# Kernel tuning notes

Measured on AMD Instinct MI355X. Metric: run time of the kernel, lower is better.

The kernel has to match this reference:

```python
import jax, jax.numpy as jnp
import numpy as np

# All unordered pairs of 6 ligand sites (octahedral complex)
PAIRS = np.array([(i, j) for i in range(6) for j in range(i + 1, 6)], dtype=np.int32)  # [15, 2]

B, N_LIGS, D = 32768, 6, 64
IN_DIM = D + 2 * D  # core + lig_i + lig_j = 192
H1, H2 = 64, 32


def setup_inputs() -> dict:
    key = jax.random.key(0)
    ks = jax.random.split(key, 8)
    s = 0.05  # small init scale for numerical sanity
    return {
        "core": jax.random.normal(ks[0], (B, D), dtype=jnp.float32),
        "ligs": jax.random.normal(ks[1], (B, N_LIGS, D), dtype=jnp.float32),
        "W1": jax.random.normal(ks[2], (IN_DIM, H1), dtype=jnp.float32) * s,
        "b1": jnp.zeros((H1,), dtype=jnp.float32),
        "W2": jax.random.normal(ks[3], (H1, H2), dtype=jnp.float32) * s,
        "b2": jnp.zeros((H2,), dtype=jnp.float32),
        "W3": jax.random.normal(ks[4], (H2, 1), dtype=jnp.float32) * s,
        "b3": jnp.zeros((1,), dtype=jnp.float32),
    }


def _mlp(x, W1, b1, W2, b2, W3, b3):
    # Dense(softplus) -> Dense(softplus) -> Dense(1, linear); dropout is identity at inference
    h = jax.nn.softplus(x @ W1 + b1)
    h = jax.nn.softplus(h @ W2 + b2)
    return h @ W3 + b3  # [..., 1]


def reference(core, ligs, W1, b1, W2, b2, W3, b3):
    i_idx = jnp.asarray(PAIRS[:, 0])
    j_idx = jnp.asarray(PAIRS[:, 1])
    P = PAIRS.shape[0]
    li = ligs[:, i_idx, :]  # [B, P, D]
    lj = ligs[:, j_idx, :]  # [B, P, D]
    c = jnp.broadcast_to(core[:, None, :], (core.shape[0], P, core.shape[1]))
    x1 = jnp.concatenate([c, li, lj], axis=-1)  # [B, P, 3D]
    x2 = jnp.concatenate([c, lj, li], axis=-1)  # [B, P, 3D]
    res = 0.5 * (_mlp(x1, W1, b1, W2, b2, W3, b3) + _mlp(x2, W1, b1, W2, b2, W3, b3))  # [B, P, 1]
    return jnp.sum(res, axis=1)  # [B, 1]
```

## Files before the change

### kernel.cpp

```cpp
#include <hip/hip_runtime.h>
#include <hip/hip_fp16.h>
#include <stdint.h>


typedef __attribute__((ext_vector_type(8))) _Float16 f16x8;
typedef __attribute__((ext_vector_type(2))) __fp16   fp16v2;
typedef __attribute__((ext_vector_type(4))) float    f32x4;
typedef __attribute__((ext_vector_type(4))) unsigned int u32x4;

constexpr int   BPB      = 64;
constexpr int   NT       = 1024;
constexpr int   T_STRIDE = 1680;
constexpr int   WT_RS    = 72;
constexpr int   WT_OFF   = BPB * T_STRIDE;
constexpr int   W2T_OFF  = WT_OFF + 192 * WT_RS * 2;
constexpr int   Y_OFF    = W2T_OFF + 32 * WT_RS * 2;
constexpr int   LDS_BYTES = Y_OFF + 256;

constexpr float L2E = 1.4426950408889634f;
constexpr float LN2 = 0.6931471805599453f;

constexpr unsigned long long I_BITS =
  (0ull<<0)|(0ull<<3)|(0ull<<6)|(0ull<<9)|(0ull<<12)|
  (1ull<<15)|(1ull<<18)|(1ull<<21)|(1ull<<24)|
  (2ull<<27)|(2ull<<30)|(2ull<<33)|
  (3ull<<36)|(3ull<<39)|(4ull<<42);
constexpr unsigned long long J_BITS =
  (1ull<<0)|(2ull<<3)|(3ull<<6)|(4ull<<9)|(5ull<<12)|
  (2ull<<15)|(3ull<<18)|(4ull<<21)|(5ull<<24)|
  (3ull<<27)|(4ull<<30)|(5ull<<33)|
  (4ull<<36)|(5ull<<39)|(5ull<<42);

__device__ __forceinline__ float sp2(float s) {
  float t = __builtin_amdgcn_exp2f(s);
  return __builtin_amdgcn_logf(1.0f + t);
}

__device__ __forceinline__ __half2 h1pair(__half2 u, __half2 a, __half2 b,
                                          __half2 one2) {
  __half2 s = __hadd2(__hadd2(u, a), b);
  __half2 t = h2exp2(s);
  return h2log2(__hadd2(one2, t));
}

__global__ __launch_bounds__(NT, 4)
void tb_fused(const float* __restrict__ core, const float* __restrict__ ligs,
              const float* __restrict__ W1,   const float* __restrict__ b1,
              const float* __restrict__ W2,   const float* __restrict__ b2,
              const float* __restrict__ W3,   const float* __restrict__ b3,
              float* __restrict__ out)
{
  extern __shared__ char smem[];
  const int tid  = (int)threadIdx.x;
  const int lane = tid & 63;
  const int ln   = lane & 15;
  const int qd   = lane >> 4;
  const int wv   = __builtin_amdgcn_readfirstlane(tid >> 6);
  const int qr   = wv >> 2;
  const int mtw  = wv & 3;
  const int b0   = (int)blockIdx.x * BPB;

  float* yred = (float*)(smem + Y_OFF);

  #pragma unroll 4
  for (int idx = tid; idx < 12288; idx += NT) {
    const int d = idx >> 6, n = idx & 63;
    *(uint16_t*)(smem + WT_OFF + ((((d >> 6) * 64 + n) * WT_RS + (d & 63)) * 2)) =
        __half_as_ushort(__float2half(W1[idx] * L2E));
  }
  #pragma unroll
  for (int idx = tid; idx < 2048; idx += NT) {
    const int k = idx >> 5, m = idx & 31;
    *(uint16_t*)(smem + W2T_OFF + ((m * WT_RS + k) * 2)) =
        __half_as_ushort(__float2half(W2[idx]));
  }
  if (tid < 64) yred[tid] = 0.0f;
  __syncthreads();

  #pragma unroll 1
  for (int rep = 0; rep < 2; ++rep) {
    const int xr = qr + rep * 4;
    if (xr >= 7) break;
    const float* src = (xr == 0)
        ? (core + (size_t)(b0 + mtw * 16 + ln) * 64)
        : (ligs + ((size_t)(b0 + mtw * 16 + ln) * 6 + (size_t)(xr - 1)) * 64);

    union AF { f16x8 v; fp16v2 p[4]; } Afr[2];
    #pragma unroll
    for (int ks = 0; ks < 2; ++ks) {
      const float4 f0 = *(const float4*)(src + ks * 32 + qd * 8);
      const float4 f1 = *(const float4*)(src + ks * 32 + qd * 8 + 4);
      Afr[ks].p[0] = __builtin_amdgcn_cvt_pkrtz(f0.x, f0.y);
      Afr[ks].p[1] = __builtin_amdgcn_cvt_pkrtz(f0.z, f0.w);
      Afr[ks].p[2] = __builtin_amdgcn_cvt_pkrtz(f1.x, f1.y);
      Afr[ks].p[3] = __builtin_amdgcn_cvt_pkrtz(f1.z, f1.w);
    }

    const int sl_lo = (xr == 0) ? 0 : 1;
    const int sl_hi = (xr == 0) ? 0 : 2;
    #pragma unroll 1
    for (int sl = sl_lo; sl <= sl_hi; ++sl) {
      const int trow = (xr == 0) ? 0 : ((sl == 1) ? xr : 6 + xr);
      #pragma unroll
      for (int nt = 0; nt < 4; ++nt) {
        f32x4 c = {0.f, 0.f, 0.f, 0.f};
        #pragma unroll
        for (int ks = 0; ks < 2; ++ks) {
          f16x8 Bf = *(const f16x8*)(smem + WT_OFF +
              (((sl * 64 + nt * 16 + ln) * WT_RS + ks * 32 + qd * 8) * 2));
          c = __builtin_amdgcn_mfma_f32_16x16x32_f16(Afr[ks].v, Bf, c, 0, 0, 0);
        }
        const float bias = (xr == 0) ? b1[nt * 16 + ln] * L2E : 0.0f;
        #pragma unroll
        for (int reg = 0; reg < 4; ++reg) {
          const int b = mtw * 16 + qd * 4 + reg;
          *(uint16_t*)(smem + (size_t)b * T_STRIDE + trow * 128 + (nt * 16 + ln) * 2) =
              __half_as_ushort(__float2half(c[reg] + bias));
        }
      }
    }
  }
  __syncthreads();

  f16x8 W2f[2][2];
  #pragma unroll
  for (int nt = 0; nt < 2; ++nt)
    #pragma unroll
    for (int ks = 0; ks < 2; ++ks)
      W2f[nt][ks] = *(const f16x8*)(smem + W2T_OFF +
          (((nt * 16 + ln) * WT_RS + ks * 32 + qd * 8) * 2));

  float b2v[2], w3v[2];
  #pragma unroll
  for (int nt = 0; nt < 2; ++nt) {
    b2v[nt] = b2[nt * 16 + ln] * L2E;
    w3v[nt] = W3[nt * 16 + ln] * LN2;
  }

  const __half2 one2 = __float2half2_rn(1.0f);
  const char* Tb  = smem + (size_t)(mtw * 16 + ln) * T_STRIDE;
  const int koff  = qd * 16;

  float yacc[4] = {0.f, 0.f, 0.f, 0.f};

  #pragma unroll 2
  for (int t3 = 0; t3 < 8; ++t3) {
    const int q = qr + 4 * t3;
    if (q >= 30) break;
    const int p  = q >> 1;
    const int iv = (int)((I_BITS >> (3 * p)) & 7ull);
    const int jv = (int)((J_BITS >> (3 * p)) & 7ull);
    const int An = (q & 1) ? jv : iv;
    const int Bn = (q & 1) ? iv : jv;
    const char* TA = Tb + (1 + An) * 128;
    const char* TB = Tb + (7 + Bn) * 128;

    union U4 { u32x4 u; __half2 h[4]; };
    U4 du0, da0, db0, du1, da1, db1;
    du0.u = *(const u32x4*)(Tb + koff);
    da0.u = *(const u32x4*)(TA + koff);
    db0.u = *(const u32x4*)(TB + koff);
    du1.u = *(const u32x4*)(Tb + 64 + koff);
    da1.u = *(const u32x4*)(TA + 64 + koff);
    db1.u = *(const u32x4*)(TB + 64 + koff);

    union { f16x8 v; __half2 h[4]; } A0, A1;
    #pragma unroll
    for (int w = 0; w < 4; ++w) A0.h[w] = h1pair(du0.h[w], da0.h[w], db0.h[w], one2);
    #pragma unroll
    for (int w = 0; w < 4; ++w) A1.h[w] = h1pair(du1.h[w], da1.h[w], db1.h[w], one2);

    f32x4 c0 = {0.f, 0.f, 0.f, 0.f};
    f32x4 c1 = {0.f, 0.f, 0.f, 0.f};
    c0 = __builtin_amdgcn_mfma_f32_16x16x32_f16(A0.v, W2f[0][0], c0, 0, 0, 0);
    c0 = __builtin_amdgcn_mfma_f32_16x16x32_f16(A1.v, W2f[0][1], c0, 0, 0, 0);
    c1 = __builtin_amdgcn_mfma_f32_16x16x32_f16(A0.v, W2f[1][0], c1, 0, 0, 0);
    c1 = __builtin_amdgcn_mfma_f32_16x16x32_f16(A1.v, W2f[1][1], c1, 0, 0, 0);

    #pragma unroll
    for (int reg = 0; reg < 4; ++reg) {
      yacc[reg] += sp2(c0[reg] + b2v[0]) * w3v[0]
                 + sp2(c1[reg] + b2v[1]) * w3v[1];
    }
  }

  #pragma unroll
  for (int reg = 0; reg < 4; ++reg) {
    float v = yacc[reg];
    v += __shfl_xor(v, 1);
    v += __shfl_xor(v, 2);
    v += __shfl_xor(v, 4);
    v += __shfl_xor(v, 8);
    yacc[reg] = v;
  }
  if (ln == 0) {
    #pragma unroll
    for (int reg = 0; reg < 4; ++reg)
      atomicAdd(&yred[mtw * 16 + qd * 4 + reg], yacc[reg]);
  }
  __syncthreads();
  if (tid < 64) out[b0 + tid] = 0.5f * yred[tid] + 15.0f * b3[0];
}

extern "C" void kernel_launch(void* const* d_in, const int* in_sizes, int n_in,
                              void* d_out, int out_size, void* d_ws, size_t ws_size,
                              hipStream_t stream) {
  const float* core = (const float*)d_in[0];
  const float* ligs = (const float*)d_in[1];
  const float* W1   = (const float*)d_in[2];
  const float* b1   = (const float*)d_in[3];
  const float* W2   = (const float*)d_in[4];
  const float* b2   = (const float*)d_in[5];
  const float* W3   = (const float*)d_in[6];
  const float* b3   = (const float*)d_in[7];
  float* out = (float*)d_out;

  const int B = in_sizes[0] / 64;
  const int grid = B / BPB;

  (void)hipFuncSetAttribute((const void*)tb_fused,
                            hipFuncAttributeMaxDynamicSharedMemorySize, LDS_BYTES);

  tb_fused<<<dim3(grid), dim3(NT), LDS_BYTES, stream>>>(
      core, ligs, W1, b1, W2, b2, W3, b3, out);
}
```

Before: 126.9 us.

## Move weight conversion to a prep kernel and halve batch per block

A separate prep kernel converts W1/W2 to transposed, pre-scaled fp16 and stores them with biases in workspace. The main kernel no longer stages weights in LDS: it reads MFMA B-fragments straight from global/L2, which drops one block barrier and frees LDS. The batch per block is halved to 32 with a new wave-to-tile mapping so that more blocks fit per CU (launch bounds now ask for 8). The costs are repeated global weight-fragment loads per wave, a second kernel launch, and the first-layer weight preprocessing being redone on every call.

```diff
diff --git a/kernel.cpp b/kernel.cpp
--- a/kernel.cpp
+++ b/kernel.cpp
@@ -8,14 +8,18 @@
 typedef __attribute__((ext_vector_type(4))) float    f32x4;
 typedef __attribute__((ext_vector_type(4))) unsigned int u32x4;
 
-constexpr int   BPB      = 64;
-constexpr int   NT       = 1024;
-constexpr int   T_STRIDE = 1680;
-constexpr int   WT_RS    = 72;
-constexpr int   WT_OFF   = BPB * T_STRIDE;
-constexpr int   W2T_OFF  = WT_OFF + 192 * WT_RS * 2;
-constexpr int   Y_OFF    = W2T_OFF + 32 * WT_RS * 2;
-constexpr int   LDS_BYTES = Y_OFF + 256;
+constexpr int   BPB       = 32;
+constexpr int   NT        = 1024;
+constexpr int   T_STRIDE  = 1680;
+constexpr int   Y_OFF     = BPB * T_STRIDE;
+constexpr int   LDS_BYTES = Y_OFF + 128;
+
+constexpr int   WS_W1T   = 0;
+constexpr int   WS_W2T   = 24576;
+constexpr int   WS_B1    = 28672;
+constexpr int   WS_B2    = 28928;
+constexpr int   WS_W3    = 29056;
+constexpr int   WS_BYTES = 29184;
 
 constexpr float L2E = 1.4426950408889634f;
 constexpr float LN2 = 0.6931471805599453f;
@@ -43,11 +47,38 @@
   return h2log2(__hadd2(one2, t));
 }
 
-__global__ __launch_bounds__(NT, 4)
+__global__ __launch_bounds__(256)
+void prep(const float* __restrict__ W1, const float* __restrict__ b1,
+          const float* __restrict__ W2, const float* __restrict__ b2,
+          const float* __restrict__ W3, char* __restrict__ ws)
+{
+  const int t = (int)(blockIdx.x * blockDim.x + threadIdx.x);
+  uint16_t* w1t = (uint16_t*)(ws + WS_W1T);
+  uint16_t* w2t = (uint16_t*)(ws + WS_W2T);
+  float*    b1s = (float*)(ws + WS_B1);
+  float*    b2s = (float*)(ws + WS_B2);
+  float*    w3s = (float*)(ws + WS_W3);
+  if (t < 12288) {
+    const int d = t >> 6, n = t & 63;
+    const int slab = d >> 6;
+    w1t[(slab * 64 + n) * 64 + (d & 63)] =
+        __half_as_ushort(__float2half(W1[t] * L2E));
+  } else if (t < 14336) {
+    const int e = t - 12288;
+    const int k = e >> 5, m = e & 31;
+    w2t[m * 64 + k] = __half_as_ushort(__float2half(W2[e]));
+  } else if (t < 14400) {
+    b1s[t - 14336] = b1[t - 14336] * L2E;
+  } else if (t < 14432) {
+    b2s[t - 14400] = b2[t - 14400] * L2E;
+  } else if (t < 14464) {
+    w3s[t - 14432] = W3[t - 14432] * LN2;
+  }
+}
+
+__global__ __launch_bounds__(NT, 8)
 void tb_fused(const float* __restrict__ core, const float* __restrict__ ligs,
-              const float* __restrict__ W1,   const float* __restrict__ b1,
-              const float* __restrict__ W2,   const float* __restrict__ b2,
-              const float* __restrict__ W3,   const float* __restrict__ b3,
+              const float* __restrict__ b3,   const char* __restrict__ ws,
               float* __restrict__ out)
 {
   extern __shared__ char smem[];
@@ -56,34 +87,29 @@
   const int ln   = lane & 15;
   const int qd   = lane >> 4;
   const int wv   = __builtin_amdgcn_readfirstlane(tid >> 6);
-  const int qr   = wv >> 2;
-  const int mtw  = wv & 3;
   const int b0   = (int)blockIdx.x * BPB;
 
+  const uint16_t* w1t = (const uint16_t*)(ws + WS_W1T);
+  const uint16_t* w2t = (const uint16_t*)(ws + WS_W2T);
+  const float*    b1s = (const float*)(ws + WS_B1);
+  const float*    b2s = (const float*)(ws + WS_B2);
+  const float*    w3s = (const float*)(ws + WS_W3);
+
   float* yred = (float*)(smem + Y_OFF);
-
-  #pragma unroll 4
-  for (int idx = tid; idx < 12288; idx += NT) {
-    const int d = idx >> 6, n = idx & 63;
-    *(uint16_t*)(smem + WT_OFF + ((((d >> 6) * 64 + n) * WT_RS + (d & 63)) * 2)) =
-        __half_as_ushort(__float2half(W1[idx] * L2E));
-  }
-  #pragma unroll
-  for (int idx = tid; idx < 2048; idx += NT) {
-    const int k = idx >> 5, m = idx & 31;
-    *(uint16_t*)(smem + W2T_OFF + ((m * WT_RS + k) * 2)) =
-        __half_as_ushort(__float2half(W2[idx]));
-  }
-  if (tid < 64) yred[tid] = 0.0f;
-  __syncthreads();
+  if (tid < BPB) yred[tid] = 0.0f;
 
   #pragma unroll 1
-  for (int rep = 0; rep < 2; ++rep) {
-    const int xr = qr + rep * 4;
-    if (xr >= 7) break;
+  for (int jj = 0; jj < 2; ++jj) {
+    const int j = wv + 16 * jj;
+    if (j >= 26) break;
+    int xr, sl, mt, trow;
+    if (j < 2)  { xr = 0; sl = 0; mt = j; trow = 0; }
+    else        { const int e = j - 2; xr = (e >> 2) + 1; sl = 1 + ((e >> 1) & 1);
+                  mt = e & 1; trow = (sl == 1) ? xr : 6 + xr; }
+
     const float* src = (xr == 0)
-        ? (core + (size_t)(b0 + mtw * 16 + ln) * 64)
-        : (ligs + ((size_t)(b0 + mtw * 16 + ln) * 6 + (size_t)(xr - 1)) * 64);
+        ? (core + (size_t)(b0 + mt * 16 + ln) * 64)
+        : (ligs + ((size_t)(b0 + mt * 16 + ln) * 6 + (size_t)(xr - 1)) * 64);
 
     union AF { f16x8 v; fp16v2 p[4]; } Afr[2];
     #pragma unroll
@@ -96,47 +122,42 @@
       Afr[ks].p[3] = __builtin_amdgcn_cvt_pkrtz(f1.z, f1.w);
     }
 
-    const int sl_lo = (xr == 0) ? 0 : 1;
-    const int sl_hi = (xr == 0) ? 0 : 2;
-    #pragma unroll 1
-    for (int sl = sl_lo; sl <= sl_hi; ++sl) {
-      const int trow = (xr == 0) ? 0 : ((sl == 1) ? xr : 6 + xr);
+    #pragma unroll
+    for (int nt = 0; nt < 4; ++nt) {
+      f32x4 c = {0.f, 0.f, 0.f, 0.f};
       #pragma unroll
-      for (int nt = 0; nt < 4; ++nt) {
-        f32x4 c = {0.f, 0.f, 0.f, 0.f};
-        #pragma unroll
-        for (int ks = 0; ks < 2; ++ks) {
-          f16x8 Bf = *(const f16x8*)(smem + WT_OFF +
-              (((sl * 64 + nt * 16 + ln) * WT_RS + ks * 32 + qd * 8) * 2));
-          c = __builtin_amdgcn_mfma_f32_16x16x32_f16(Afr[ks].v, Bf, c, 0, 0, 0);
-        }
-        const float bias = (xr == 0) ? b1[nt * 16 + ln] * L2E : 0.0f;
-        #pragma unroll
-        for (int reg = 0; reg < 4; ++reg) {
-          const int b = mtw * 16 + qd * 4 + reg;
-          *(uint16_t*)(smem + (size_t)b * T_STRIDE + trow * 128 + (nt * 16 + ln) * 2) =
-              __half_as_ushort(__float2half(c[reg] + bias));
-        }
+      for (int ks = 0; ks < 2; ++ks) {
+        const f16x8 Bf = *(const f16x8*)(w1t +
+            (sl * 64 + nt * 16 + ln) * 64 + ks * 32 + qd * 8);
+        c = __builtin_amdgcn_mfma_f32_16x16x32_f16(Afr[ks].v, Bf, c, 0, 0, 0);
+      }
+      const float bias = (trow == 0) ? b1s[nt * 16 + ln] : 0.0f;
+      #pragma unroll
+      for (int reg = 0; reg < 4; ++reg) {
+        const int b = mt * 16 + qd * 4 + reg;
+        *(uint16_t*)(smem + (size_t)b * T_STRIDE + trow * 128 + (nt * 16 + ln) * 2) =
+            __half_as_ushort(__float2half(c[reg] + bias));
       }
     }
   }
-  __syncthreads();
 
   f16x8 W2f[2][2];
   #pragma unroll
   for (int nt = 0; nt < 2; ++nt)
     #pragma unroll
     for (int ks = 0; ks < 2; ++ks)
-      W2f[nt][ks] = *(const f16x8*)(smem + W2T_OFF +
-          (((nt * 16 + ln) * WT_RS + ks * 32 + qd * 8) * 2));
-
+      W2f[nt][ks] = *(const f16x8*)(w2t + (nt * 16 + ln) * 64 + ks * 32 + qd * 8);
   float b2v[2], w3v[2];
   #pragma unroll
   for (int nt = 0; nt < 2; ++nt) {
-    b2v[nt] = b2[nt * 16 + ln] * L2E;
-    w3v[nt] = W3[nt * 16 + ln] * LN2;
-  }
-
+    b2v[nt] = b2s[nt * 16 + ln];
+    w3v[nt] = w3s[nt * 16 + ln];
+  }
+
+  __syncthreads();
+
+  const int mtw = wv & 1;
+  const int qr  = wv >> 1;
   const __half2 one2 = __float2half2_rn(1.0f);
   const char* Tb  = smem + (size_t)(mtw * 16 + ln) * T_STRIDE;
   const int koff  = qd * 16;
@@ -144,8 +165,8 @@
   float yacc[4] = {0.f, 0.f, 0.f, 0.f};
 
   #pragma unroll 2
-  for (int t3 = 0; t3 < 8; ++t3) {
-    const int q = qr + 4 * t3;
+  for (int t3 = 0; t3 < 4; ++t3) {
+    const int q = qr + 8 * t3;
     if (q >= 30) break;
     const int p  = q >> 1;
     const int iv = (int)((I_BITS >> (3 * p)) & 7ull);
@@ -199,7 +220,7 @@
       atomicAdd(&yred[mtw * 16 + qd * 4 + reg], yacc[reg]);
   }
   __syncthreads();
-  if (tid < 64) out[b0 + tid] = 0.5f * yred[tid] + 15.0f * b3[0];
+  if (tid < BPB) out[b0 + tid] = 0.5f * yred[tid] + 15.0f * b3[0];
 }
 
 extern "C" void kernel_launch(void* const* d_in, const int* in_sizes, int n_in,
@@ -214,13 +235,15 @@
   const float* W3   = (const float*)d_in[6];
   const float* b3   = (const float*)d_in[7];
   float* out = (float*)d_out;
+  char*  ws  = (char*)d_ws;
 
   const int B = in_sizes[0] / 64;
   const int grid = B / BPB;
 
+  prep<<<dim3(57), dim3(256), 0, stream>>>(W1, b1, W2, b2, W3, ws);
+
   (void)hipFuncSetAttribute((const void*)tb_fused,
                             hipFuncAttributeMaxDynamicSharedMemorySize, LDS_BYTES);
-
   tb_fused<<<dim3(grid), dim3(NT), LDS_BYTES, stream>>>(
-      core, ligs, W1, b1, W2, b2, W3, b3, out);
-}
+      core, ligs, b3, ws, out);
+}
```

Result: slower. 146.5 us (+15.5%).
